# Optimization experiments

Hardware: AMD Instinct MI355X
Metric: run time of the kernel (lower is better)

## Reference

```python
import jax, jax.numpy as jnp
import numpy as np

B, LF, RATE = 2, 2048, 4
DF, DS, H = 1024, 1024, 8
D2 = DF // 2            # 512: both self (d1) and cross (d2) branch dims (equal split)
POOL_H = 2048
TS = LF // RATE         # 512 slow steps


def _p(key, shape):
    return jax.random.normal(key, shape, jnp.float32) * 0.02


def setup_inputs() -> dict:
    keys = iter(jax.random.split(jax.random.key(0), 32))
    inp = {
        "x_fast": jax.random.normal(next(keys), (B, LF, DF), jnp.float32),
        "x_slow": jax.random.normal(next(keys), (B, TS, DS), jnp.float32),
    }
    for name in ("fself", "fcross", "sself", "scross"):
        inp[f"{name}_wqkv"] = _p(next(keys), (D2, 3 * D2))
        inp[f"{name}_bqkv"] = jnp.zeros((3 * D2,), jnp.float32)
        inp[f"{name}_wo"] = _p(next(keys), (D2, D2))
        inp[f"{name}_bo"] = jnp.zeros((D2,), jnp.float32)
    inp["lift_w"] = _p(next(keys), (DS, D2))
    inp["lift_b"] = jnp.zeros((D2,), jnp.float32)
    inp["pool_w1"] = _p(next(keys), (RATE * DF, POOL_H))
    inp["pool_b1"] = jnp.zeros((POOL_H,), jnp.float32)
    inp["pool_w2"] = _p(next(keys), (POOL_H, D2))
    inp["pool_b2"] = jnp.zeros((D2,), jnp.float32)
    return inp


def _mha(q_in, k_in, v_in, wqkv, bqkv, wo, bo):
    """Standard multihead attention with fused in-proj weight [d, 3d]."""
    b, tq, d = q_in.shape
    hd = d // H
    q = q_in @ wqkv[:, :d] + bqkv[:d]
    k = k_in @ wqkv[:, d:2 * d] + bqkv[d:2 * d]
    v = v_in @ wqkv[:, 2 * d:] + bqkv[2 * d:]
    q = q.reshape(b, tq, H, hd)
    k = k.reshape(b, k_in.shape[1], H, hd)
    v = v.reshape(b, v_in.shape[1], H, hd)
    scores = jnp.einsum('bqhd,bkhd->bhqk', q, k) * np.float32(1.0 / np.sqrt(hd))
    w = jax.nn.softmax(scores, axis=-1)
    o = jnp.einsum('bhqk,bkhd->bqhd', w, v).reshape(b, tq, d)
    return o @ wo + bo


def _forward(x_fast, x_slow,
             fself_wqkv, fself_bqkv, fself_wo, fself_bo,
             fcross_wqkv, fcross_bqkv, fcross_wo, fcross_bo,
             sself_wqkv, sself_bqkv, sself_wo, sself_bo,
             scross_wqkv, scross_bqkv, scross_wo, scross_bo,
             lift_w, lift_b, pool_w1, pool_b1, pool_w2, pool_b2):
    b = x_fast.shape[0]
    # ---- fast level: lift slow -> fast timescale (ffn applied before repeat)
    y = jnp.repeat(x_slow @ lift_w + lift_b, RATE, axis=1)          # [B, LF, D2]
    x1, x2 = x_fast[..., :D2], x_fast[..., D2:]
    z_fast = jnp.concatenate([
        _mha(x1, x1, x1, fself_wqkv, fself_bqkv, fself_wo, fself_bo),
        _mha(x2, y, y, fcross_wqkv, fcross_bqkv, fcross_wo, fcross_bo),
    ], axis=-1)
    # ---- slow level: causal block pooling of fast sequence
    blocks = x_fast.reshape(b, TS, RATE * DF)                        # LF == TS*RATE
    s = jax.nn.gelu(blocks @ pool_w1 + pool_b1) @ pool_w2 + pool_b2  # [B, TS, D2]
    # causal shift: prepend zero slow step, drop last (zero in pooled feature dim)
    s = jnp.concatenate([jnp.zeros((b, 1, D2), s.dtype), s[:, :-1]], axis=1)
    s1, s2 = x_slow[..., :D2], x_slow[..., D2:]
    z_slow = jnp.concatenate([
        _mha(s1, s1, s1, sself_wqkv, sself_bqkv, sself_wo, sself_bo),
        _mha(s2, s, s, scross_wqkv, scross_bqkv, scross_wo, scross_bo),
    ], axis=-1)
    return z_fast, z_slow


def reference(x_fast, x_slow,
              fself_wqkv, fself_bqkv, fself_wo, fself_bo,
              fcross_wqkv, fcross_bqkv, fcross_wo, fcross_bo,
              sself_wqkv, sself_bqkv, sself_wo, sself_bo,
              scross_wqkv, scross_bqkv, scross_wo, scross_bo,
              lift_w, lift_b, pool_w1, pool_b1, pool_w2, pool_b2):
    return _forward(x_fast, x_slow,
                    fself_wqkv, fself_bqkv, fself_wo, fself_bo,
                    fcross_wqkv, fcross_bqkv, fcross_wo, fcross_bo,
                    sself_wqkv, sself_bqkv, sself_wo, sself_bo,
                    scross_wqkv, scross_bqkv, scross_wo, scross_bo,
                    lift_w, lift_b, pool_w1, pool_b1, pool_w2, pool_b2)
```

## Files before the change

kernel.cpp:

```cpp
#include <hip/hip_runtime.h>
#include <hip/hip_bf16.h>


typedef __attribute__((ext_vector_type(8))) short bf16x8;
typedef __attribute__((ext_vector_type(4))) float f32x4;
typedef unsigned short u16;
typedef unsigned int u32;

__device__ inline u16 f2bf(float f) {
    __hip_bfloat16 h = __float2bfloat16(f);
    return *reinterpret_cast<u16*>(&h);
}
__device__ inline u32 pack2(float a, float b) {
    return (u32)f2bf(a) | ((u32)f2bf(b) << 16);
}
__device__ inline float bf2f(u16 h) {
    u32 x = ((u32)h) << 16; float f;
    __builtin_memcpy(&f, &x, 4);
    return f;
}
__device__ inline void gld16(const u16* g, u16* l) {
    __builtin_amdgcn_global_load_lds(
        (const __attribute__((address_space(1))) void*)(g),
        (__attribute__((address_space(3))) void*)(l), 16, 0, 0);
}

struct GDesc {
    const u16* A; const u16* Bt; const float* bias;
    void* out0; u16* aux0; u16* aux1;
    int lda, ldb, ldc, K, ntx, mode, rshift, tile_end;
};
struct GPack { int n; int pad[3]; GDesc d[8]; };

template <int TMT>
__global__ __launch_bounds__(256)
void gemm_multi(GPack pk)
{
    constexpr int TM = TMT * 16;
    constexpr int W = TMT / 2;
    constexpr int BUF = TM * 64;
    __shared__ u16 As[2 * BUF];
    __shared__ u16 Bs[2 * BUF];

    int bid = blockIdx.x;
    int di = 0;
    while (bid >= pk.d[di].tile_end) ++di;
    const GDesc g = pk.d[di];
    const int base = di ? pk.d[di - 1].tile_end : 0;
    const int local = bid - base;
    const int ty = local / g.ntx, tx = local - ty * g.ntx;
    const int row0 = ty * TM, col0 = tx * TM;

    const int t = threadIdx.x;
    const int wave = t >> 6, lane = t & 63;
    const int l15 = lane & 15, quad = lane >> 4;
    const int wm = (wave >> 1) * W * 16, wn = (wave & 1) * W * 16;

    const int srow = wave * 8 + (lane >> 3);
    const int ssw = (((lane & 7) ^ (lane >> 3))) * 8;
    const u16* Ag = g.A + (long long)(row0 + srow) * g.lda + ssw;
    const u16* Bg = g.Bt + (long long)(col0 + srow) * g.ldb + ssw;

    const int c0 = (quad ^ (l15 & 7)) * 8;

    f32x4 acc[W][W];
#pragma unroll
    for (int i = 0; i < W; ++i)
#pragma unroll
        for (int j = 0; j < W; ++j) {
            acc[i][j][0] = 0.f; acc[i][j][1] = 0.f;
            acc[i][j][2] = 0.f; acc[i][j][3] = 0.f;
        }

    auto stage = [&](int buf, int k0) {
#pragma unroll
        for (int r = 0; r < TM / 32; ++r) {
            gld16(Ag + (long long)r * 32 * g.lda + k0, As + buf * BUF + r * 2048 + wave * 512);
            gld16(Bg + (long long)r * 32 * g.ldb + k0, Bs + buf * BUF + r * 2048 + wave * 512);
        }
    };
    auto compute = [&](int buf) {
        const u16* Ab = As + buf * BUF;
        const u16* Bb = Bs + buf * BUF;
#pragma unroll
        for (int kc = 0; kc < 2; ++kc) {
            const int cc = kc ? (c0 ^ 32) : c0;
            bf16x8 af[W], bfr[W];
#pragma unroll
            for (int i = 0; i < W; ++i) {
                af[i]  = *(const bf16x8*)(Ab + (wm + i * 16 + l15) * 64 + cc);
                bfr[i] = *(const bf16x8*)(Bb + (wn + i * 16 + l15) * 64 + cc);
            }
#pragma unroll
            for (int i = 0; i < W; ++i)
#pragma unroll
                for (int j = 0; j < W; ++j)
                    acc[i][j] = __builtin_amdgcn_mfma_f32_16x16x32_bf16(af[i], bfr[j], acc[i][j], 0, 0, 0);
        }
    };

    stage(0, 0);
    __syncthreads();
    const int npairs = g.K >> 7;
    int k0 = 64;
    for (int s = 0; s < npairs - 1; ++s) {
        stage(1, k0);       compute(0); __syncthreads();
        stage(0, k0 + 64);  compute(1); __syncthreads();
        k0 += 128;
    }
    stage(1, k0); compute(0); __syncthreads();
    compute(1);

    const int rmask = (1 << g.rshift) - 1;
#pragma unroll
    for (int i = 0; i < W; ++i)
#pragma unroll
        for (int j = 0; j < W; ++j)
#pragma unroll
            for (int r = 0; r < 4; ++r) {
                int m = row0 + wm + i * 16 + quad * 4 + r;
                int n = col0 + wn + j * 16 + l15;
                float v = acc[i][j][r];
                if (g.mode != 5) v += g.bias[n];
                if (g.mode == 0) {
                    ((float*)g.out0)[(long long)m * g.ldc + n] = v;
                } else if (g.mode == 1 || g.mode == 5) {
                    ((u16*)g.out0)[(long long)m * g.ldc + n] = f2bf(v);
                } else if (g.mode == 2) {
                    float x3 = v * v * v;
                    v = 0.5f * v * (1.f + tanhf(0.7978845608028654f * (v + 0.044715f * x3)));
                    ((u16*)g.out0)[(long long)m * g.ldc + n] = f2bf(v);
                } else if (g.mode == 3) {
                    u16 h = f2bf(v);
                    if (n < 512) ((u16*)g.out0)[(long long)m * 512 + n] = h;
                    else if (n < 1024) g.aux0[(long long)m * 512 + (n - 512)] = h;
                    else {
                        int d = n - 1024;
                        int bb = m >> g.rshift, rr = m & rmask;
                        g.aux1[((long long)((bb * 8 + (d >> 6)) * 64 + (d & 63)) << g.rshift) + rr] = h;
                    }
                } else if (g.mode == 4) {
                    u16 h = f2bf(v);
                    if (n < 512) ((u16*)g.out0)[(long long)m * 512 + n] = h;
                    else {
                        int d = n - 512;
                        int bb = m >> g.rshift, rr = m & rmask;
                        g.aux1[((long long)((bb * 8 + (d >> 6)) * 64 + (d & 63)) << g.rshift) + rr] = h;
                    }
                } else {
                    int t9 = m & 511;
                    if (t9 != 511) ((u16*)g.out0)[(long long)(m + 1) * g.ldc + n] = f2bf(v);
                    if (t9 == 0)  ((u16*)g.out0)[(long long)m * g.ldc + n] = 0;
                }
            }
}

#define ALD 72

struct ADesc { const u16* Q; const u16* K; const u16* Vt; u16* O; int Rq, nk, tile_end, pad; };
struct APack { int n; int pad[3]; ADesc d[4]; };

__global__ __launch_bounds__(256)
void attn_multi(APack pk, float prescale)
{
    __shared__ u16 Ks[2 * 64 * 64];
    __shared__ u16 Vts[2 * 64 * 64];
    __shared__ u16 Ps[4][16 * ALD];

    int bid = blockIdx.x;
    int di = 0;
    while (bid >= pk.d[di].tile_end) ++di;
    const ADesc g = pk.d[di];
    const int base = di ? pk.d[di - 1].tile_end : 0;
    const int local = bid - base;

    const int t = threadIdx.x;
    const int wave = t >> 6, lane = t & 63;
    const int l15 = lane & 15, quad = lane >> 4;
    const int bh = local & 15, b = bh >> 3, h = bh & 7;
    const int q0 = (local >> 4) * 64;
    const int nk = g.nk;

    const int srow = wave * 8 + (lane >> 3);
    const int ssw = (((lane & 7) ^ (lane >> 3))) * 8;
    const int c0 = (quad ^ (l15 & 7)) * 8;

    const u16* Qg = g.Q + ((long long)(b * g.Rq + q0 + srow) << 9) + h * 64 + ssw;
    const u16* Kg = g.K + ((long long)(b * nk + srow) << 9) + h * 64 + ssw;
    const u16* Vg = g.Vt + (long long)bh * 64 * nk + (long long)srow * nk + ssw;

#pragma unroll
    for (int r = 0; r < 2; ++r)
        gld16(Qg + ((long long)r * 32 << 9), Ks + 4096 + r * 2048 + wave * 512);
    __syncthreads();

    bf16x8 qf[2];
    qf[0] = *(const bf16x8*)(Ks + 4096 + (wave * 16 + l15) * 64 + c0);
    qf[1] = *(const bf16x8*)(Ks + 4096 + (wave * 16 + l15) * 64 + (c0 ^ 32));

    f32x4 Oacc[4];
#pragma unroll
    for (int nt = 0; nt < 4; ++nt) { Oacc[nt][0] = 0.f; Oacc[nt][1] = 0.f; Oacc[nt][2] = 0.f; Oacc[nt][3] = 0.f; }
    float lr[4] = {0.f, 0.f, 0.f, 0.f};

    u16* Pw = &Ps[wave][0];

    auto stage = [&](int buf, int kt) {
#pragma unroll
        for (int r = 0; r < 2; ++r) {
            gld16(Kg + ((long long)(kt + r * 32) << 9), Ks + buf * 4096 + r * 2048 + wave * 512);
            gld16(Vg + (long long)r * 32 * nk + kt, Vts + buf * 4096 + r * 2048 + wave * 512);
        }
    };
    auto acompute = [&](int buf) {
        const u16* Kb = Ks + buf * 4096;
        const u16* Vb = Vts + buf * 4096;
#pragma unroll
        for (int k16 = 0; k16 < 4; ++k16) {
            f32x4 s;
            s[0] = 0.f; s[1] = 0.f; s[2] = 0.f; s[3] = 0.f;
            bf16x8 kf0 = *(const bf16x8*)(Kb + (k16 * 16 + l15) * 64 + c0);
            bf16x8 kf1 = *(const bf16x8*)(Kb + (k16 * 16 + l15) * 64 + (c0 ^ 32));
            s = __builtin_amdgcn_mfma_f32_16x16x32_bf16(qf[0], kf0, s, 0, 0, 0);
            s = __builtin_amdgcn_mfma_f32_16x16x32_bf16(qf[1], kf1, s, 0, 0, 0);
#pragma unroll
            for (int r = 0; r < 4; ++r) {
                float p = exp2f(s[r] * prescale);
                lr[r] += p;
                Pw[(quad * 4 + r) * ALD + k16 * 16 + l15] = f2bf(p);
            }
        }
        bf16x8 pf0 = *(const bf16x8*)(Pw + l15 * ALD + quad * 8);
        bf16x8 pf1 = *(const bf16x8*)(Pw + l15 * ALD + 32 + quad * 8);
#pragma unroll
        for (int nt = 0; nt < 4; ++nt) {
            bf16x8 vf0 = *(const bf16x8*)(Vb + (nt * 16 + l15) * 64 + c0);
            bf16x8 vf1 = *(const bf16x8*)(Vb + (nt * 16 + l15) * 64 + (c0 ^ 32));
            Oacc[nt] = __builtin_amdgcn_mfma_f32_16x16x32_bf16(pf0, vf0, Oacc[nt], 0, 0, 0);
            Oacc[nt] = __builtin_amdgcn_mfma_f32_16x16x32_bf16(pf1, vf1, Oacc[nt], 0, 0, 0);
        }
    };

    stage(0, 0);
    __syncthreads();
    const int npairs = nk >> 7;
    int kt = 64;
    for (int s2 = 0; s2 < npairs - 1; ++s2) {
        stage(1, kt);       acompute(0); __syncthreads();
        stage(0, kt + 64);  acompute(1); __syncthreads();
        kt += 128;
    }
    stage(1, kt); acompute(0); __syncthreads();
    acompute(1);

    float inv[4];
#pragma unroll
    for (int r = 0; r < 4; ++r) {
        float s = lr[r];
#pragma unroll
        for (int off = 1; off < 16; off <<= 1) s += __shfl_xor(s, off);
        inv[r] = 1.f / s;
    }

    u16* Ob = g.O + ((long long)(b * g.Rq + q0 + wave * 16 + quad * 4) << 9) + h * 64;
#pragma unroll
    for (int nt = 0; nt < 4; ++nt)
#pragma unroll
        for (int r = 0; r < 4; ++r)
            Ob[(long long)r * 512 + nt * 16 + l15] = f2bf(Oacc[nt][r] * inv[r]);
}

struct WDesc { const float* src; u16* dst; int ldn, K, tx_, tile_end; };
struct WPack { int n; int pad[3]; WDesc d[12]; };

__global__ __launch_bounds__(256)
void wt_multi(WPack pk)
{
    __shared__ float T[64][68];
    int bid = blockIdx.x;
    int di = 0;
    while (bid >= pk.d[di].tile_end) ++di;
    const WDesc g = pk.d[di];
    const int base = di ? pk.d[di - 1].tile_end : 0;
    const int local = bid - base;
    const int k0 = (local % g.tx_) * 64;
    const int n0 = (local / g.tx_) * 64;
    const int t = threadIdx.x;
#pragma unroll
    for (int i = 0; i < 4; ++i) {
        int idx = t + i * 256;
        int r = idx >> 4, c4 = idx & 15;
        float4 v = *(const float4*)(g.src + (long long)(k0 + r) * g.ldn + n0 + c4 * 4);
        T[r][c4 * 4 + 0] = v.x; T[r][c4 * 4 + 1] = v.y;
        T[r][c4 * 4 + 2] = v.z; T[r][c4 * 4 + 3] = v.w;
    }
    __syncthreads();
#pragma unroll
    for (int i = 0; i < 4; ++i) {
        int idx = t + i * 256;
        int rn = idx >> 4, k4 = idx & 15;
        uint2 u;
        u.x = pack2(T[k4 * 4 + 0][rn], T[k4 * 4 + 1][rn]);
        u.y = pack2(T[k4 * 4 + 2][rn], T[k4 * 4 + 3][rn]);
        *(uint2*)(g.dst + (long long)(n0 + rn) * g.K + k0 + k4 * 4) = u;
    }
}

__global__ __launch_bounds__(256)
void c_cvt2(const float* __restrict__ a, u16* __restrict__ da, int na8,
            const float* __restrict__ b, u16* __restrict__ db)
{
    int i = blockIdx.x * 256 + threadIdx.x;
    const float* s; u16* d;
    if (i < na8) { s = a + (long long)i * 8; d = da + (long long)i * 8; }
    else { s = b + (long long)(i - na8) * 8; d = db + (long long)(i - na8) * 8; }
    float4 x = *(const float4*)s;
    float4 y = *(const float4*)(s + 4);
    uint4 u;
    u.x = pack2(x.x, x.y); u.y = pack2(x.z, x.w);
    u.z = pack2(y.x, y.y); u.w = pack2(y.z, y.w);
    *(uint4*)d = u;
}

__global__ __launch_bounds__(256)
void gelu_sum(u16* __restrict__ p0, const u16* __restrict__ p1,
              const float* __restrict__ bias)
{
    int i8 = (blockIdx.x * 256 + threadIdx.x) * 8;
    uint4 a = *(const uint4*)(p0 + i8);
    uint4 b = *(const uint4*)(p1 + i8);
    int n = i8 & 2047;
    float4 bi0 = *(const float4*)(bias + n);
    float4 bi1 = *(const float4*)(bias + n + 4);
    float bb[8] = {bi0.x, bi0.y, bi0.z, bi0.w, bi1.x, bi1.y, bi1.z, bi1.w};
    u32 aw[4] = {a.x, a.y, a.z, a.w};
    u32 bw[4] = {b.x, b.y, b.z, b.w};
    u32 ow[4];
#pragma unroll
    for (int k = 0; k < 4; ++k) {
        float v0 = bf2f((u16)(aw[k] & 0xffff)) + bf2f((u16)(bw[k] & 0xffff)) + bb[2 * k];
        float v1 = bf2f((u16)(aw[k] >> 16)) + bf2f((u16)(bw[k] >> 16)) + bb[2 * k + 1];
        float x3 = v0 * v0 * v0;
        v0 = 0.5f * v0 * (1.f + tanhf(0.7978845608028654f * (v0 + 0.044715f * x3)));
        x3 = v1 * v1 * v1;
        v1 = 0.5f * v1 * (1.f + tanhf(0.7978845608028654f * (v1 + 0.044715f * x3)));
        ow[k] = pack2(v0, v1);
    }
    uint4 o; o.x = ow[0]; o.y = ow[1]; o.z = ow[2]; o.w = ow[3];
    *(uint4*)(p0 + i8) = o;
}

extern "C" void kernel_launch(void* const* d_in, const int* in_sizes, int n_in,
                              void* d_out, int out_size, void* d_ws, size_t ws_size,
                              hipStream_t stream)
{
    const float* x_fast      = (const float*)d_in[0];
    const float* x_slow      = (const float*)d_in[1];
    const float* fself_wqkv  = (const float*)d_in[2];
    const float* fself_bqkv  = (const float*)d_in[3];
    const float* fself_wo    = (const float*)d_in[4];
    const float* fself_bo    = (const float*)d_in[5];
    const float* fcross_wqkv = (const float*)d_in[6];
    const float* fcross_bqkv = (const float*)d_in[7];
    const float* fcross_wo   = (const float*)d_in[8];
    const float* fcross_bo   = (const float*)d_in[9];
    const float* sself_wqkv  = (const float*)d_in[10];
    const float* sself_bqkv  = (const float*)d_in[11];
    const float* sself_wo    = (const float*)d_in[12];
    const float* sself_bo    = (const float*)d_in[13];
    const float* scross_wqkv = (const float*)d_in[14];
    const float* scross_bqkv = (const float*)d_in[15];
    const float* scross_wo   = (const float*)d_in[16];
    const float* scross_bo   = (const float*)d_in[17];
    const float* lift_w      = (const float*)d_in[18];
    const float* lift_b      = (const float*)d_in[19];
    const float* pool_w1     = (const float*)d_in[20];
    const float* pool_b1     = (const float*)d_in[21];
    const float* pool_w2     = (const float*)d_in[22];
    const float* pool_b2     = (const float*)d_in[23];

    float* out = (float*)d_out;
    float* zf = out;
    float* zs = out + 2LL * 2048 * 1024;

    float* ws = (float*)d_ws;
    u16* pw1T     = (u16*)(ws + 0);
    u16* wqkvT_f  = (u16*)(ws + 4194304);
    u16* wqkvT_c  = (u16*)(ws + 4587520);
    u16* wqkvT_s  = (u16*)(ws + 4980736);
    u16* wqkvT_sc = (u16*)(ws + 5373952);
    u16* liftT    = (u16*)(ws + 5767168);
    u16* pw2T     = (u16*)(ws + 6029312);
    u16* woT_f    = (u16*)(ws + 6553600);
    u16* woT_c    = (u16*)(ws + 6684672);
    u16* woT_s    = (u16*)(ws + 6815744);
    u16* woT_sc   = (u16*)(ws + 6946816);
    u16* xfb      = (u16*)(ws + 7077888);
    u16* xsb      = (u16*)(ws + 9175040);
    u16* q1       = (u16*)(ws + 9699328);
    u16* k1       = (u16*)(ws + 10747904);
    u16* vt1      = (u16*)(ws + 11796480);
    u16* qs       = (u16*)(ws + 12845056);
    u16* ks       = (u16*)(ws + 13107200);
    u16* vts      = (u16*)(ws + 13369344);
    u16* qcs      = (u16*)(ws + 13631488);
    u16* k2    = (u16*)(ws + 0);
    u16* vt2   = (u16*)(ws + 262144);
    u16* sbufS = (u16*)(ws + 524288);
    u16* kcs   = (u16*)(ws + 786432);
    u16* vtcs  = (u16*)(ws + 1048576);
    u16* fo1   = (u16*)(ws + 1310720);
    u16* fo2   = (u16*)(ws + 2359296);
    u16* so1   = (u16*)(ws + 3407872);
    u16* so2   = (u16*)(ws + 3670016);
    u16* q2   = (u16*)(out + 0);
    u16* ybuf = (u16*)(out + 1048576);
    u16* hbuf = (u16*)(out + 1310720);
    u16* p1b  = (u16*)(out + 2359296);

    hipLaunchKernelGGL(c_cvt2, dim3(2560), dim3(256), 0, stream,
                       x_fast, xfb, 524288, x_slow, xsb);

    {
        WPack p; p.n = 11;
        int te = 0, i = 0;
        auto add = [&](const float* s, u16* d, int ldn, int K, int N) {
            te += (K / 64) * (N / 64);
            p.d[i++] = WDesc{s, d, ldn, K, K / 64, te};
        };
        add(pool_w1, pw1T, 2048, 4096, 2048);
        add(fself_wqkv, wqkvT_f, 1536, 512, 1536);
        add(fcross_wqkv, wqkvT_c, 1536, 512, 1536);
        add(sself_wqkv, wqkvT_s, 1536, 512, 1536);
        add(scross_wqkv, wqkvT_sc, 1536, 512, 1536);
        add(lift_w, liftT, 512, 1024, 512);
        add(pool_w2, pw2T, 512, 2048, 512);
        add(fself_wo, woT_f, 512, 512, 512);
        add(fcross_wo, woT_c, 512, 512, 512);
        add(sself_wo, woT_s, 512, 512, 512);
        add(scross_wo, woT_sc, 512, 512, 512);
        hipLaunchKernelGGL(wt_multi, dim3(te), dim3(256), 0, stream, p);
    }

    auto gl = [&](GPack& p, int i, const u16* A, int lda,
                  const u16* Bt, int ldb, const float* bias,
                  void* out0, int ldc, int M, int N, int K, int mode,
                  u16* aux0, u16* aux1, int rshift, int TM, int& te) {
        te += (M / TM) * (N / TM);
        p.d[i] = GDesc{A, Bt, bias, out0, aux0, aux1,
                       lda, ldb, ldc, K, N / TM, mode, rshift, te};
    };

    {
        GPack p; p.n = 7; int te = 0;
        gl(p, 0, xfb, 4096, pw1T, 4096, pool_b1, hbuf, 2048,
           1024, 2048, 2048, 5, 0, 0, 0, 128, te);
        gl(p, 1, xfb + 2048, 4096, pw1T + 2048, 4096, pool_b1, p1b, 2048,
           1024, 2048, 2048, 5, 0, 0, 0, 128, te);
        gl(p, 2, xfb, 1024, wqkvT_f, 512, fself_bqkv, q1, 512,
           4096, 1536, 512, 3, k1, vt1, 11, 128, te);
        gl(p, 3, xfb + 512, 1024, wqkvT_c, 512, fcross_bqkv, q2, 512,
           4096, 512, 512, 1, 0, 0, 0, 128, te);
        gl(p, 4, xsb, 1024, wqkvT_s, 512, sself_bqkv, qs, 512,
           1024, 1536, 512, 3, ks, vts, 9, 128, te);
        gl(p, 5, xsb, 1024, liftT, 1024, lift_b, ybuf, 512,
           1024, 512, 1024, 1, 0, 0, 0, 128, te);
        gl(p, 6, xsb + 512, 1024, wqkvT_sc, 512, scross_bqkv, qcs, 512,
           1024, 512, 512, 1, 0, 0, 0, 128, te);
        hipLaunchKernelGGL(gemm_multi<8>, dim3(te), dim3(256), 0, stream, p);
    }

    hipLaunchKernelGGL(gelu_sum, dim3(1024), dim3(256), 0, stream, hbuf, p1b, pool_b1);

    {
        GPack p; p.n = 2; int te = 0;
        gl(p, 0, ybuf, 512, wqkvT_c + 512 * 512, 512, fcross_bqkv + 512, k2, 512,
           1024, 1024, 512, 4, 0, vt2, 9, 64, te);
        gl(p, 1, hbuf, 2048, pw2T, 2048, pool_b2, sbufS, 512,
           1024, 512, 2048, 6, 0, 0, 0, 64, te);
        hipLaunchKernelGGL(gemm_multi<4>, dim3(te), dim3(256), 0, stream, p);
    }

    {
        GPack p; p.n = 1; int te = 0;
        gl(p, 0, sbufS, 512, wqkvT_sc + 512 * 512, 512, scross_bqkv + 512, kcs, 512,
           1024, 1024, 512, 4, 0, vtcs, 9, 64, te);
        hipLaunchKernelGGL(gemm_multi<4>, dim3(te), dim3(256), 0, stream, p);
    }

    {
        APack p; p.n = 4;
        int te = 0, i = 0;
        auto add = [&](const u16* Q, const u16* K, const u16* Vt, u16* O, int Rq, int nk) {
            te += (Rq / 64) * 16;
            p.d[i++] = ADesc{Q, K, Vt, O, Rq, nk, te, 0};
        };
        add(q1, k1, vt1, fo1, 2048, 2048);
        add(q2, k2, vt2, fo2, 2048, 512);
        add(qs, ks, vts, so1, 512, 512);
        add(qcs, kcs, vtcs, so2, 512, 512);
        hipLaunchKernelGGL(attn_multi, dim3(te), dim3(256), 0, stream, p,
                           0.125f * 1.4426950408889634f);
    }

    {
        GPack p; p.n = 4; int te = 0;
        gl(p, 0, fo1, 512, woT_f, 512, fself_bo, zf, 1024,
           4096, 512, 512, 0, 0, 0, 0, 128, te);
        gl(p, 1, fo2, 512, woT_c, 512, fcross_bo, zf + 512, 1024,
           4096, 512, 512, 0, 0, 0, 0, 128, te);
        gl(p, 2, so1, 512, woT_s, 512, sself_bo, zs, 1024,
           1024, 512, 512, 0, 0, 0, 0, 128, te);
        gl(p, 3, so2, 512, woT_sc, 512, scross_bo, zs + 512, 1024,
           1024, 512, 512, 0, 0, 0, 0, 128, te);
        hipLaunchKernelGGL(gemm_multi<8>, dim3(te), dim3(256), 0, stream, p);
    }
}
```

Before: 364.3 us.

## Pipeline GEMM and attention K-loops with partial vmcnt waits and raw barriers

Rewrites the double-buffered main loops of the GEMM and attention kernels so the next tile's global-to-LDS load is issued before waiting. Each step then waits with a partial s_waitcnt vmcnt, so only the current tile's loads must land and the prefetch stays in flight. Raw s_barrier calls with sched_barrier fences replace __syncthreads. The attention kernel gets its own Q LDS buffer so the Q load overlaps the first K/V stage. This relies on hand-counted vmcnt values matching the number of issued loads, which is fragile if the load count or the compiler's instruction order changes.

```diff
diff --git a/kernel.cpp b/kernel.cpp
--- a/kernel.cpp
+++ b/kernel.cpp
@@ -23,6 +23,12 @@
     __builtin_amdgcn_global_load_lds(
         (const __attribute__((address_space(1))) void*)(g),
         (__attribute__((address_space(3))) void*)(l), 16, 0, 0);
+}
+template <int N>
+__device__ inline void wait_vmcnt() {
+    if constexpr (N == 0)      asm volatile("s_waitcnt vmcnt(0)" ::: "memory");
+    else if constexpr (N == 4) asm volatile("s_waitcnt vmcnt(4)" ::: "memory");
+    else if constexpr (N == 8) asm volatile("s_waitcnt vmcnt(8)" ::: "memory");
 }
 
 struct GDesc {
@@ -39,6 +45,7 @@
     constexpr int TM = TMT * 16;
     constexpr int W = TMT / 2;
     constexpr int BUF = TM * 64;
+    constexpr int NLD = TM / 32 * 2;
     __shared__ u16 As[2 * BUF];
     __shared__ u16 Bs[2 * BUF];
 
@@ -99,17 +106,23 @@
         }
     };
 
+    const int nt = g.K >> 6;
     stage(0, 0);
-    __syncthreads();
-    const int npairs = g.K >> 7;
-    int k0 = 64;
-    for (int s = 0; s < npairs - 1; ++s) {
-        stage(1, k0);       compute(0); __syncthreads();
-        stage(0, k0 + 64);  compute(1); __syncthreads();
-        k0 += 128;
-    }
-    stage(1, k0); compute(0); __syncthreads();
-    compute(1);
+    for (int tt = 0; tt < nt; ++tt) {
+        const int cur = tt & 1;
+        if (tt + 1 < nt) {
+            stage(cur ^ 1, (tt + 1) << 6);
+            wait_vmcnt<NLD>();
+        } else {
+            wait_vmcnt<0>();
+        }
+        __builtin_amdgcn_sched_barrier(0);
+        __builtin_amdgcn_s_barrier();
+        __builtin_amdgcn_sched_barrier(0);
+        compute(cur);
+        __builtin_amdgcn_sched_barrier(0);
+        __builtin_amdgcn_s_barrier();
+    }
 
     const int rmask = (1 << g.rshift) - 1;
 #pragma unroll
@@ -163,6 +176,7 @@
 __global__ __launch_bounds__(256)
 void attn_multi(APack pk, float prescale)
 {
+    __shared__ u16 Qs[64 * 64];
     __shared__ u16 Ks[2 * 64 * 64];
     __shared__ u16 Vts[2 * 64 * 64];
     __shared__ u16 Ps[4][16 * ALD];
@@ -189,22 +203,6 @@
     const u16* Kg = g.K + ((long long)(b * nk + srow) << 9) + h * 64 + ssw;
     const u16* Vg = g.Vt + (long long)bh * 64 * nk + (long long)srow * nk + ssw;
 
-#pragma unroll
-    for (int r = 0; r < 2; ++r)
-        gld16(Qg + ((long long)r * 32 << 9), Ks + 4096 + r * 2048 + wave * 512);
-    __syncthreads();
-
-    bf16x8 qf[2];
-    qf[0] = *(const bf16x8*)(Ks + 4096 + (wave * 16 + l15) * 64 + c0);
-    qf[1] = *(const bf16x8*)(Ks + 4096 + (wave * 16 + l15) * 64 + (c0 ^ 32));
-
-    f32x4 Oacc[4];
-#pragma unroll
-    for (int nt = 0; nt < 4; ++nt) { Oacc[nt][0] = 0.f; Oacc[nt][1] = 0.f; Oacc[nt][2] = 0.f; Oacc[nt][3] = 0.f; }
-    float lr[4] = {0.f, 0.f, 0.f, 0.f};
-
-    u16* Pw = &Ps[wave][0];
-
     auto stage = [&](int buf, int kt) {
 #pragma unroll
         for (int r = 0; r < 2; ++r) {
@@ -212,6 +210,27 @@
             gld16(Vg + (long long)r * 32 * nk + kt, Vts + buf * 4096 + r * 2048 + wave * 512);
         }
     };
+
+#pragma unroll
+    for (int r = 0; r < 2; ++r)
+        gld16(Qg + ((long long)r * 32 << 9), Qs + r * 2048 + wave * 512);
+    stage(0, 0);
+    wait_vmcnt<4>();
+    __builtin_amdgcn_sched_barrier(0);
+    __builtin_amdgcn_s_barrier();
+    __builtin_amdgcn_sched_barrier(0);
+
+    bf16x8 qf[2];
+    qf[0] = *(const bf16x8*)(Qs + (wave * 16 + l15) * 64 + c0);
+    qf[1] = *(const bf16x8*)(Qs + (wave * 16 + l15) * 64 + (c0 ^ 32));
+
+    f32x4 Oacc[4];
+#pragma unroll
+    for (int nt2 = 0; nt2 < 4; ++nt2) { Oacc[nt2][0] = 0.f; Oacc[nt2][1] = 0.f; Oacc[nt2][2] = 0.f; Oacc[nt2][3] = 0.f; }
+    float lr[4] = {0.f, 0.f, 0.f, 0.f};
+
+    u16* Pw = &Ps[wave][0];
+
     auto acompute = [&](int buf) {
         const u16* Kb = Ks + buf * 4096;
         const u16* Vb = Vts + buf * 4096;
@@ -233,25 +252,30 @@
         bf16x8 pf0 = *(const bf16x8*)(Pw + l15 * ALD + quad * 8);
         bf16x8 pf1 = *(const bf16x8*)(Pw + l15 * ALD + 32 + quad * 8);
 #pragma unroll
-        for (int nt = 0; nt < 4; ++nt) {
-            bf16x8 vf0 = *(const bf16x8*)(Vb + (nt * 16 + l15) * 64 + c0);
-            bf16x8 vf1 = *(const bf16x8*)(Vb + (nt * 16 + l15) * 64 + (c0 ^ 32));
-            Oacc[nt] = __builtin_amdgcn_mfma_f32_16x16x32_bf16(pf0, vf0, Oacc[nt], 0, 0, 0);
-            Oacc[nt] = __builtin_amdgcn_mfma_f32_16x16x32_bf16(pf1, vf1, Oacc[nt], 0, 0, 0);
+        for (int nt2 = 0; nt2 < 4; ++nt2) {
+            bf16x8 vf0 = *(const bf16x8*)(Vb + (nt2 * 16 + l15) * 64 + c0);
+            bf16x8 vf1 = *(const bf16x8*)(Vb + (nt2 * 16 + l15) * 64 + (c0 ^ 32));
+            Oacc[nt2] = __builtin_amdgcn_mfma_f32_16x16x32_bf16(pf0, vf0, Oacc[nt2], 0, 0, 0);
+            Oacc[nt2] = __builtin_amdgcn_mfma_f32_16x16x32_bf16(pf1, vf1, Oacc[nt2], 0, 0, 0);
         }
     };
 
-    stage(0, 0);
-    __syncthreads();
-    const int npairs = nk >> 7;
-    int kt = 64;
-    for (int s2 = 0; s2 < npairs - 1; ++s2) {
-        stage(1, kt);       acompute(0); __syncthreads();
-        stage(0, kt + 64);  acompute(1); __syncthreads();
-        kt += 128;
-    }
-    stage(1, kt); acompute(0); __syncthreads();
-    acompute(1);
+    const int nt = nk >> 6;
+    for (int tt = 0; tt < nt; ++tt) {
+        const int cur = tt & 1;
+        if (tt + 1 < nt) {
+            stage(cur ^ 1, (tt + 1) << 6);
+            wait_vmcnt<4>();
+        } else {
+            wait_vmcnt<0>();
+        }
+        __builtin_amdgcn_sched_barrier(0);
+        __builtin_amdgcn_s_barrier();
+        __builtin_amdgcn_sched_barrier(0);
+        acompute(cur);
+        __builtin_amdgcn_sched_barrier(0);
+        __builtin_amdgcn_s_barrier();
+    }
 
     float inv[4];
 #pragma unroll
@@ -264,10 +288,10 @@
 
     u16* Ob = g.O + ((long long)(b * g.Rq + q0 + wave * 16 + quad * 4) << 9) + h * 64;
 #pragma unroll
-    for (int nt = 0; nt < 4; ++nt)
+    for (int nt2 = 0; nt2 < 4; ++nt2)
 #pragma unroll
         for (int r = 0; r < 4; ++r)
-            Ob[(long long)r * 512 + nt * 16 + l15] = f2bf(Oacc[nt][r] * inv[r]);
+            Ob[(long long)r * 512 + nt2 * 16 + l15] = f2bf(Oacc[nt2][r] * inv[r]);
 }
 
 struct WDesc { const float* src; u16* dst; int ldn, K, tx_, tile_end; };
```

New measurement: 359.9 us. Within noise of the previous version (-1.2%).
